# Performance work log

Hardware: AMD Instinct MI355X
Metric: run time of the kernel (lower is better)

The kernel has to match this reference:

```python
import jax, jax.numpy as jnp
import numpy as np

FEAT_DIM = 512
NUM_HEADS = 8
HEAD_DIM = FEAT_DIM // NUM_HEADS


def setup_inputs() -> dict:
    key = jax.random.key(0)
    ks = jax.random.split(key, 10)
    B, T, D = 4, 2048, FEAT_DIM
    scale = 1.0 / np.sqrt(D)
    inp = {
        "x_current": jax.random.normal(ks[0], (B, T, D), jnp.float32),
        "x_past": jax.random.normal(ks[1], (B, T, D), jnp.float32),
        "wq": jax.random.normal(ks[2], (D, D), jnp.float32) * scale,
        "bq": jnp.zeros((D,), jnp.float32),
        "wk": jax.random.normal(ks[3], (D, D), jnp.float32) * scale,
        "bk": jnp.zeros((D,), jnp.float32),
        "wv": jax.random.normal(ks[4], (D, D), jnp.float32) * scale,
        "bv": jnp.zeros((D,), jnp.float32),
        "wo": jax.random.normal(ks[5], (D, D), jnp.float32) * scale,
        "bo": jnp.zeros((D,), jnp.float32),
    }
    return inp


def reference(x_current, x_past, wq, bq, wk, bk, wv, bv, wo, bo):
    B, T, D = x_current.shape
    H, Hd = NUM_HEADS, HEAD_DIM
    # QKV projections (torch Linear: x @ W.T + b)
    Q = (x_current @ wq.T + bq).reshape(B, T, H, Hd).transpose(0, 2, 1, 3)
    K = (x_past @ wk.T + bk).reshape(B, T, H, Hd).transpose(0, 2, 1, 3)
    V = (x_past @ wv.T + bv).reshape(B, T, H, Hd).transpose(0, 2, 1, 3)
    # scaled dot-product attention, full T x T scores as in the original
    scores = jnp.einsum("bhqd,bhkd->bhqk", Q, K) / jnp.sqrt(jnp.asarray(Hd, Q.dtype))
    attn = jax.nn.softmax(scores, axis=-1)
    out = jnp.einsum("bhqk,bhkd->bhqd", attn, V)
    out = out.transpose(0, 2, 1, 3).reshape(B, T, D)
    return out @ wo.T + bo
```

## Files before the change

### kernel.cpp

```cpp
#include <hip/hip_runtime.h>
#include <math.h>

#define BATCH 4
#define SEQ 2048
#define FEAT 512
#define NHEADS 8
#define HD 64
#define NROWS (BATCH*SEQ)
#define QSCALE 0.18033688011112042f

typedef __attribute__((ext_vector_type(4)))  float f32x4;
typedef __attribute__((ext_vector_type(16))) float f32x16;
typedef __attribute__((ext_vector_type(8)))  short s16x8;
typedef __attribute__((ext_vector_type(8)))  unsigned short u16x8;
typedef __attribute__((ext_vector_type(4)))  unsigned int u32x4;

#if __has_builtin(__builtin_amdgcn_exp2f)
#define EX2(x) __builtin_amdgcn_exp2f(x)
#else
#define EX2(x) __expf((x) * 0.6931471805599453f)
#endif

static __device__ __forceinline__ unsigned short f2bf(float x) {
  unsigned int u = __builtin_bit_cast(unsigned int, x);
  unsigned int r = (u + 0x7FFFu + ((u >> 16) & 1u)) >> 16;
  return (unsigned short)r;
}
static __device__ __forceinline__ float bf2f(unsigned short h) {
  unsigned int u = ((unsigned int)h) << 16;
  return __builtin_bit_cast(float, u);
}
static __device__ __forceinline__ void split2(float x, unsigned short& h, unsigned short& l) {
  h = f2bf(x);
  l = f2bf(x - bf2f(h));
}

static __device__ __forceinline__ void glds16(const unsigned short* g, unsigned short* l) {
  __builtin_amdgcn_global_load_lds(
      (const __attribute__((address_space(1))) unsigned int*)g,
      (__attribute__((address_space(3))) unsigned int*)l,
      16, 0, 0);
}

__global__ __launch_bounds__(256) void presplit(
    const float* __restrict__ wq, const float* __restrict__ wk,
    const float* __restrict__ wv, const float* __restrict__ wo,
    const float* __restrict__ xc, const float* __restrict__ xp,
    unsigned short* __restrict__ Wsp,
    unsigned short* __restrict__ Xchi, unsigned short* __restrict__ Xphi)
{
  const int bid = blockIdx.x;
  if (bid < 512) {
    const int mat = bid >> 7;
    const int chunk = ((bid & 127) * 256 + threadIdx.x) * 8;
    const float* src = (mat == 0) ? wq : (mat == 1) ? wk : (mat == 2) ? wv : wo;
    unsigned short* hi = Wsp + (size_t)mat * 524288;
    unsigned short* lo = hi + 262144;
    const f32x4 a = *reinterpret_cast<const f32x4*>(&src[chunk]);
    const f32x4 b = *reinterpret_cast<const f32x4*>(&src[chunk + 4]);
    u16x8 h8, l8;
#pragma unroll
    for (int i = 0; i < 4; ++i) { unsigned short hh, ll; split2(a[i], hh, ll); h8[i] = hh; l8[i] = ll; }
#pragma unroll
    for (int i = 0; i < 4; ++i) { unsigned short hh, ll; split2(b[i], hh, ll); h8[4 + i] = hh; l8[4 + i] = ll; }
    *reinterpret_cast<u16x8*>(&hi[chunk]) = h8;
    *reinterpret_cast<u16x8*>(&lo[chunk]) = l8;
  } else {
    const int i = bid - 512;
    const int half = i >> 11;
    const int ib = i & 2047;
    const float* src = half ? xp : xc;
    unsigned short* dst = half ? Xphi : Xchi;
    const int chunk = (ib * 256 + threadIdx.x) * 8;
    const f32x4 a = *reinterpret_cast<const f32x4*>(&src[chunk]);
    const f32x4 b = *reinterpret_cast<const f32x4*>(&src[chunk + 4]);
    u16x8 h8;
#pragma unroll
    for (int ii = 0; ii < 4; ++ii) h8[ii] = f2bf(a[ii]);
#pragma unroll
    for (int ii = 0; ii < 4; ++ii) h8[4 + ii] = f2bf(b[ii]);
    *reinterpret_cast<u16x8*>(&dst[chunk]) = h8;
  }
}

__global__ __launch_bounds__(256, 4) void qkv_proj(
    const unsigned short* __restrict__ Xchi, const unsigned short* __restrict__ Xphi,
    const unsigned short* __restrict__ Wsp,
    const float* __restrict__ bq, const float* __restrict__ bk,
    const float* __restrict__ bv,
    unsigned short* __restrict__ Qhi, unsigned short* __restrict__ Khi,
    unsigned short* __restrict__ Vthi)
{
  __shared__ unsigned short Xh[128 * 64];
  __shared__ unsigned short Whi[64 * 64], Wlo[64 * 64];

  const int z = blockIdx.z;
  const unsigned short* Xsrc = (z == 0) ? Xchi : Xphi;
  const unsigned short* Wh_g = Wsp + (size_t)z * 524288;
  const unsigned short* Wl_g = Wh_g + 262144;
  const float* Bp = (z == 0) ? bq : (z == 1) ? bk : bv;
  const float scale = (z == 0) ? QSCALE : 1.0f;

  const int tid  = threadIdx.x;
  const int lane = tid & 63;
  const int wave = tid >> 6;
  const int g = lane >> 4, j = lane & 15;
  const int wm = (wave >> 1) * 64;
  const int wn = (wave & 1) * 32;
  const int row0 = blockIdx.x * 128;
  const int col0 = blockIdx.y * 64;

  f32x4 acc[4][2];
#pragma unroll
  for (int mi = 0; mi < 4; ++mi)
#pragma unroll
    for (int ni = 0; ni < 2; ++ni) acc[mi][ni] = (f32x4)0.f;

  const int xrow = wave * 32 + (lane >> 3);
  const int xkg  = (lane & 7) ^ ((lane >> 3) & 7);
  const unsigned short* srcX = Xsrc + (size_t)(row0 + xrow) * FEAT + xkg * 8;
  const int wrow = wave * 16 + (lane >> 3);
  const unsigned short* srcWh = Wh_g + (size_t)(col0 + wrow) * FEAT + xkg * 8;
  const unsigned short* srcWl = Wl_g + (size_t)(col0 + wrow) * FEAT + xkg * 8;

  for (int kt = 0; kt < FEAT; kt += 64) {
    __syncthreads();
#pragma unroll
    for (int c = 0; c < 4; ++c)
      glds16(srcX + kt + c * 4096, &Xh[(wave * 32 + c * 8) * 64]);
    glds16(srcWh + kt,        &Whi[(wave * 16) * 64]);
    glds16(srcWh + kt + 4096, &Whi[(wave * 16 + 8) * 64]);
    glds16(srcWl + kt,        &Wlo[(wave * 16) * 64]);
    glds16(srcWl + kt + 4096, &Wlo[(wave * 16 + 8) * 64]);
    asm volatile("s_waitcnt vmcnt(0)" ::: "memory");
    __syncthreads();

#pragma unroll
    for (int c = 0; c < 2; ++c) {
      const int koff = c * 32 + g * 8;
      s16x8 ah[4], bh[2], bl[2];
#pragma unroll
      for (int mi = 0; mi < 4; ++mi) {
        const int r = wm + mi * 16 + j;
        const int el = r * 64 + (koff ^ ((r & 7) << 3));
        ah[mi] = *reinterpret_cast<const s16x8*>(&Xh[el]);
      }
#pragma unroll
      for (int ni = 0; ni < 2; ++ni) {
        const int r = wn + ni * 16 + j;
        const int el = r * 64 + (koff ^ ((r & 7) << 3));
        bh[ni] = *reinterpret_cast<const s16x8*>(&Whi[el]);
        bl[ni] = *reinterpret_cast<const s16x8*>(&Wlo[el]);
      }
#pragma unroll
      for (int mi = 0; mi < 4; ++mi)
#pragma unroll
        for (int ni = 0; ni < 2; ++ni) {
          acc[mi][ni] = __builtin_amdgcn_mfma_f32_16x16x32_bf16(ah[mi], bh[ni], acc[mi][ni], 0, 0, 0);
          acc[mi][ni] = __builtin_amdgcn_mfma_f32_16x16x32_bf16(ah[mi], bl[ni], acc[mi][ni], 0, 0, 0);
        }
    }
  }

  if (z < 2) {
    unsigned short* Out = (z == 0) ? Qhi : Khi;
#pragma unroll
    for (int ni = 0; ni < 2; ++ni) {
      const int colc = col0 + wn + ni * 16 + j;
      const float bj = Bp[colc];
      const int h = colc >> 6, hd = colc & 63;
#pragma unroll
      for (int mi = 0; mi < 4; ++mi)
#pragma unroll
        for (int r = 0; r < 4; ++r) {
          const int rowc = row0 + wm + mi * 16 + (g << 2) + r;
          const int b = rowc >> 11, t = rowc & 2047;
          const float v = (acc[mi][ni][r] + bj) * scale;
          Out[(((size_t)b * NHEADS + h) * SEQ + t) * HD + hd] = f2bf(v);
        }
    }
  } else {
    __syncthreads();
#pragma unroll
    for (int ni = 0; ni < 2; ++ni) {
      const int hdl = wn + ni * 16 + j;
      const float bj = Bp[col0 + hdl];
#pragma unroll
      for (int mi = 0; mi < 4; ++mi)
#pragma unroll
        for (int r = 0; r < 4; ++r) {
          const int lt = wm + mi * 16 + (g << 2) + r;
          const float v = acc[mi][ni][r] + bj;
          const int el = lt * 64 + (hdl ^ ((lt & 7) << 3));
          Xh[el] = f2bf(v);
        }
    }
    __syncthreads();
    const int b = row0 >> 11, h = col0 >> 6;
    const int tbase = row0 & 2047;
#pragma unroll
    for (int c = 0; c < 4; ++c) {
      const int chunk = c * 256 + tid;
      const int hd = chunk >> 4;
      const int t0 = (chunk & 15) * 8;
      u16x8 vh;
#pragma unroll
      for (int i = 0; i < 8; ++i) {
        const int p = t0 + i;
        const int lt = (p & ~15) | ((p & 3) + (((p >> 2) & 1) << 3) + (((p >> 3) & 1) << 2));
        const int el = lt * 64 + (hd ^ ((lt & 7) << 3));
        vh[i] = Xh[el];
      }
      const size_t off = (((size_t)b * NHEADS + h) * HD + hd) * SEQ + tbase + t0;
      *reinterpret_cast<u16x8*>(&Vthi[off]) = vh;
    }
  }
}

__global__ __launch_bounds__(256, 4) void out_proj(
    const unsigned short* __restrict__ AOhi,
    const unsigned short* __restrict__ Woh,  const unsigned short* __restrict__ Wol,
    const float* __restrict__ bias, float* __restrict__ out)
{
  __shared__ unsigned short Xh[64 * 64];
  __shared__ unsigned short Whi[64 * 64], Wlo[64 * 64];

  const int tid  = threadIdx.x;
  const int lane = tid & 63;
  const int wave = tid >> 6;
  const int g = lane >> 4, j = lane & 15;
  const int wm = (wave >> 1) * 32;
  const int wn = (wave & 1) * 32;
  const int row0 = blockIdx.x * 64;
  const int col0 = blockIdx.y * 64;

  f32x4 acc[2][2];
#pragma unroll
  for (int mi = 0; mi < 2; ++mi)
#pragma unroll
    for (int ni = 0; ni < 2; ++ni) acc[mi][ni] = (f32x4)0.f;

  const int arow = wave * 16 + (lane >> 3);
  const int akg  = (lane & 7) ^ ((lane >> 3) & 7);
  const unsigned short* srcA  = AOhi + (size_t)(row0 + arow) * FEAT + akg * 8;
  const unsigned short* srcWh = Woh + (size_t)(col0 + arow) * FEAT + akg * 8;
  const unsigned short* srcWl = Wol + (size_t)(col0 + arow) * FEAT + akg * 8;

  for (int kt = 0; kt < FEAT; kt += 64) {
    __syncthreads();
    glds16(srcA + kt,         &Xh[(wave * 16) * 64]);
    glds16(srcA + kt + 4096,  &Xh[(wave * 16 + 8) * 64]);
    glds16(srcWh + kt,        &Whi[(wave * 16) * 64]);
    glds16(srcWh + kt + 4096, &Whi[(wave * 16 + 8) * 64]);
    glds16(srcWl + kt,        &Wlo[(wave * 16) * 64]);
    glds16(srcWl + kt + 4096, &Wlo[(wave * 16 + 8) * 64]);
    asm volatile("s_waitcnt vmcnt(0)" ::: "memory");
    __syncthreads();

#pragma unroll
    for (int c = 0; c < 2; ++c) {
      const int koff = c * 32 + g * 8;
      s16x8 ah[2], bh[2], bl[2];
#pragma unroll
      for (int mi = 0; mi < 2; ++mi) {
        const int r = wm + mi * 16 + j;
        const int el = r * 64 + (koff ^ ((r & 7) << 3));
        ah[mi] = *reinterpret_cast<const s16x8*>(&Xh[el]);
      }
#pragma unroll
      for (int ni = 0; ni < 2; ++ni) {
        const int r = wn + ni * 16 + j;
        const int el = r * 64 + (koff ^ ((r & 7) << 3));
        bh[ni] = *reinterpret_cast<const s16x8*>(&Whi[el]);
        bl[ni] = *reinterpret_cast<const s16x8*>(&Wlo[el]);
      }
#pragma unroll
      for (int mi = 0; mi < 2; ++mi)
#pragma unroll
        for (int ni = 0; ni < 2; ++ni) {
          acc[mi][ni] = __builtin_amdgcn_mfma_f32_16x16x32_bf16(ah[mi], bh[ni], acc[mi][ni], 0, 0, 0);
          acc[mi][ni] = __builtin_amdgcn_mfma_f32_16x16x32_bf16(ah[mi], bl[ni], acc[mi][ni], 0, 0, 0);
        }
    }
  }

#pragma unroll
  for (int ni = 0; ni < 2; ++ni) {
    const int colc = col0 + wn + ni * 16 + j;
    const float bj = bias[colc];
#pragma unroll
    for (int mi = 0; mi < 2; ++mi)
#pragma unroll
      for (int r = 0; r < 4; ++r) {
        const int rowc = row0 + wm + mi * 16 + (g << 2) + r;
        out[(size_t)rowc * FEAT + colc] = acc[mi][ni][r] + bj;
      }
  }
}

__global__ __launch_bounds__(256, 3) void attn_pipe(
    const unsigned short* __restrict__ Qhi,
    const unsigned short* __restrict__ Khi,
    const unsigned short* __restrict__ Vthi,
    unsigned short* __restrict__ AOhi)
{
  __shared__ unsigned short Kh_s[3][4096];
  __shared__ unsigned short Vh_s[3][4096];
  __shared__ float bcast[4][32];

  const int tid = threadIdx.x, lane = tid & 63, wave = tid >> 6;
  const int hfl = lane >> 5;
  const int l31 = lane & 31;

  const int bid = blockIdx.x;
  const int swz = (bid & 7) * 64 + (bid >> 3);
  const int qt  = swz & 15;
  const int bh  = swz >> 4;
  const int b = bh >> 3, h = bh & 7;

  const int q0 = qt * 128 + wave * 32;
  const size_t kvbase = (size_t)bh * SEQ * HD;

  s16x8 qh[4];
  {
    const size_t qoff = kvbase + (size_t)(q0 + l31) * HD + hfl * 8;
#pragma unroll
    for (int c = 0; c < 4; ++c)
      qh[c] = *reinterpret_cast<const s16x8*>(&Qhi[qoff + c * 16]);
  }

  f32x16 oacc0 = (f32x16)0.f, oacc1 = (f32x16)0.f;
  float m = -INFINITY, lsum = 0.f;

  const int ck  = tid >> 3;
  const int ksl = (tid & 7) ^ (ck & 7);
  const unsigned short* sKh = Khi + kvbase + (size_t)ck * HD + ksl * 8;
  const int vr  = tid >> 3;
  const int vsl = (tid & 7) ^ (vr & 7);
  const int vhd = vr + (vsl >> 2) * 32;
  const int vk0 = (vsl & 3) * 8;
  const unsigned short* sVh = Vthi + kvbase + (size_t)vhd * SEQ + vk0;
  const int wq = wave * 512;

  const int krow = l31 * 64;
  const int ksw  = l31 & 7;

  auto stage = [&](int tt, int bi) {
    const size_t ko = (size_t)tt * 64 * HD;
    const int    vo = tt * 64;
    glds16(sKh + ko,           &Kh_s[bi][wq]);
    glds16(sKh + ko + 32 * HD, &Kh_s[bi][2048 + wq]);
    glds16(sVh + vo,           &Vh_s[bi][wq]);
    glds16(sVh + vo + 32,      &Vh_s[bi][2048 + wq]);
  };

  stage(0, 0);
  stage(1, 1);

  const int NT = SEQ / 64;
  int cur = 0;
  for (int t = 0; t < NT; ++t) {
    if (t < NT - 1) {
      asm volatile("s_waitcnt vmcnt(4)" ::: "memory");
    } else {
      asm volatile("s_waitcnt vmcnt(0)" ::: "memory");
    }
    __syncthreads();
    if (t + 2 < NT) {
      int nb = cur + 2; if (nb >= 3) nb -= 3;
      stage(t + 2, nb);
    }
    __builtin_amdgcn_sched_barrier(0);

#pragma unroll
    for (int sub = 0; sub < 2; ++sub) {
      const int sb = sub * 2048;

      s16x8 KH[4];
#pragma unroll
      for (int c = 0; c < 4; ++c) {
        const int idx = sb + krow + ((((c << 1) | hfl)) ^ ksw) * 8;
        KH[c] = *reinterpret_cast<const s16x8*>(&Kh_s[cur][idx]);
      }

      f32x16 st = (f32x16)0.f;
      __builtin_amdgcn_s_setprio(1);
#pragma unroll
      for (int c = 0; c < 4; ++c)
        st = __builtin_amdgcn_mfma_f32_32x32x16_bf16(KH[c], qh[c], st, 0, 0, 0);
      __builtin_amdgcn_s_setprio(0);

      s16x8 V0h[2], V1h[2];
#pragma unroll
      for (int c = 0; c < 2; ++c) {
        const int i0 = sb + krow + ((((c << 1) | hfl)) ^ ksw) * 8;
        const int i1 = sb + krow + (((4 | (c << 1) | hfl)) ^ ksw) * 8;
        V0h[c] = *reinterpret_cast<const s16x8*>(&Vh_s[cur][i0]);
        V1h[c] = *reinterpret_cast<const s16x8*>(&Vh_s[cur][i1]);
      }

      const float a0 = fmaxf(fmaxf(st[0], st[1]), st[2]);
      const float a1 = fmaxf(fmaxf(st[3], st[4]), st[5]);
      const float a2 = fmaxf(fmaxf(st[6], st[7]), st[8]);
      const float a3 = fmaxf(fmaxf(st[9], st[10]), st[11]);
      const float a4 = fmaxf(fmaxf(st[12], st[13]), st[14]);
      const float pm = fmaxf(fmaxf(fmaxf(a0, a1), a2),
                             fmaxf(fmaxf(a3, a4), st[15]));

      if (__any(pm > m + 8.f)) {
        const float pmf  = fmaxf(pm, __shfl_xor(pm, 32));
        const float mnew = fmaxf(m, pmf);
        const float corr = EX2(m - mnew);
        m = mnew; lsum *= corr;
        if (lane < 32) bcast[wave][l31] = corr;
        f32x4 c4[4];
#pragma unroll
        for (int rq = 0; rq < 4; ++rq)
          c4[rq] = *reinterpret_cast<const f32x4*>(&bcast[wave][rq * 8 + hfl * 4]);
#pragma unroll
        for (int r = 0; r < 16; ++r) {
          const float cc = c4[r >> 2][r & 3];
          oacc0[r] *= cc; oacc1[r] *= cc;
        }
      }

#pragma unroll
      for (int r = 0; r < 16; ++r) st[r] = EX2(st[r] - m);
      {
        float s0 = (st[0] + st[1]) + (st[2] + st[3]);
        float s1 = (st[4] + st[5]) + (st[6] + st[7]);
        float s2 = (st[8] + st[9]) + (st[10] + st[11]);
        float s3 = (st[12] + st[13]) + (st[14] + st[15]);
        lsum += (s0 + s1) + (s2 + s3);
      }

      unsigned int wh[8];
#pragma unroll
      for (int p = 0; p < 8; ++p)
        asm("v_cvt_pk_bf16_f32 %0, %1, %2" : "=v"(wh[p]) : "v"(st[2 * p]), "v"(st[2 * p + 1]));
      const s16x8 pa0h = __builtin_bit_cast(s16x8, (u32x4){wh[0], wh[1], wh[2], wh[3]});
      const s16x8 pa1h = __builtin_bit_cast(s16x8, (u32x4){wh[4], wh[5], wh[6], wh[7]});

      __builtin_amdgcn_s_setprio(1);
      oacc0 = __builtin_amdgcn_mfma_f32_32x32x16_bf16(pa0h, V0h[0], oacc0, 0, 0, 0);
      oacc0 = __builtin_amdgcn_mfma_f32_32x32x16_bf16(pa1h, V0h[1], oacc0, 0, 0, 0);
      oacc1 = __builtin_amdgcn_mfma_f32_32x32x16_bf16(pa0h, V1h[0], oacc1, 0, 0, 0);
      oacc1 = __builtin_amdgcn_mfma_f32_32x32x16_bf16(pa1h, V1h[1], oacc1, 0, 0, 0);
      __builtin_amdgcn_s_setprio(0);
    }

    cur += 1; if (cur >= 3) cur -= 3;
  }

  const float lf = lsum + __shfl_xor(lsum, 32);
  if (lane < 32) bcast[wave][l31] = 1.f / lf;
  __syncthreads();
  f32x4 i4[4];
#pragma unroll
  for (int rq = 0; rq < 4; ++rq)
    i4[rq] = *reinterpret_cast<const f32x4*>(&bcast[wave][rq * 8 + hfl * 4]);

#pragma unroll
  for (int r = 0; r < 16; ++r) {
    const int q = q0 + (r & 3) + 8 * (r >> 2) + 4 * hfl;
    const float inv = i4[r >> 2][r & 3];
    const size_t idx = ((size_t)b * SEQ + q) * FEAT + h * HD + l31;
    AOhi[idx]      = f2bf(oacc0[r] * inv);
    AOhi[idx + 32] = f2bf(oacc1[r] * inv);
  }
}

extern "C" void kernel_launch(void* const* d_in, const int* in_sizes, int n_in,
                              void* d_out, int out_size, void* d_ws, size_t ws_size,
                              hipStream_t stream) {
  const float* x_cur  = (const float*)d_in[0];
  const float* x_past = (const float*)d_in[1];
  const float* wq = (const float*)d_in[2];
  const float* bq = (const float*)d_in[3];
  const float* wk = (const float*)d_in[4];
  const float* bk = (const float*)d_in[5];
  const float* wv = (const float*)d_in[6];
  const float* bv = (const float*)d_in[7];
  const float* wo = (const float*)d_in[8];
  const float* bo = (const float*)d_in[9];
  float* out = (float*)d_out;

  const size_t n = (size_t)NROWS * FEAT;
  unsigned short* Qhi  = (unsigned short*)d_ws;
  unsigned short* Xchi = Qhi + n;
  unsigned short* Khi  = Qhi + 2 * n;
  unsigned short* Xphi = Qhi + 3 * n;
  unsigned short* Vthi = Qhi + 4 * n;
  unsigned short* Wsp  = Qhi + 5 * n;
  unsigned short* AOhi = Qhi + 6 * n;

  dim3 block(256);
  presplit<<<dim3(4608), block, 0, stream>>>(wq, wk, wv, wo, x_cur, x_past,
                                             Wsp, Xchi, Xphi);

  qkv_proj<<<dim3(NROWS / 128, FEAT / 64, 3), block, 0, stream>>>(
      Xchi, Xphi, Wsp, bq, bk, bv, Qhi, Khi, Vthi);

  attn_pipe<<<dim3(512), block, 0, stream>>>(Qhi, Khi, Vthi, AOhi);

  dim3 gout(NROWS / 64, FEAT / 64);
  out_proj<<<gout, block, 0, stream>>>(AOhi, Wsp + 3 * 524288,
                                       Wsp + 3 * 524288 + 262144, bo, out);
}
```

Baseline: 103.0 us.

## Split attention over two key halves and merge partial outputs in a new kernel

The attention kernel now splits the key sequence into two halves, launching twice as many blocks, each writing unnormalized bf16 partial outputs plus per-row max and sum. A new merge kernel combines the two partials using log-sum-exp weights and writes the normalized result. The triple-buffered, two-ahead K/V prefetch is replaced by a simple double buffer with a full wait and barrier each tile. This aims to fill more CUs on a 512-block grid, at the cost of an extra kernel launch, extra memory traffic, bf16 rounding of the unnormalized partials, and less load/compute overlap.

Result: slower. 110.5 us (+7.2%).

```diff
diff --git a/kernel.cpp b/kernel.cpp
--- a/kernel.cpp
+++ b/kernel.cpp
@@ -302,17 +302,19 @@
     const unsigned short* __restrict__ Qhi,
     const unsigned short* __restrict__ Khi,
     const unsigned short* __restrict__ Vthi,
-    unsigned short* __restrict__ AOhi)
+    unsigned short* __restrict__ AOp0, unsigned short* __restrict__ AOp1,
+    float* __restrict__ ML)
 {
-  __shared__ unsigned short Kh_s[3][4096];
-  __shared__ unsigned short Vh_s[3][4096];
+  __shared__ unsigned short Kh_s[2][4096];
+  __shared__ unsigned short Vh_s[2][4096];
   __shared__ float bcast[4][32];
 
   const int tid = threadIdx.x, lane = tid & 63, wave = tid >> 6;
   const int hfl = lane >> 5;
   const int l31 = lane & 31;
 
-  const int bid = blockIdx.x;
+  const int sp  = blockIdx.x >> 9;
+  const int bid = blockIdx.x & 511;
   const int swz = (bid & 7) * 64 + (bid >> 3);
   const int qt  = swz & 15;
   const int bh  = swz >> 4;
@@ -321,6 +323,10 @@
   const int q0 = qt * 128 + wave * 32;
   const size_t kvbase = (size_t)bh * SEQ * HD;
 
+  unsigned short* AOp = sp ? AOp1 : AOp0;
+  float* mlm = ML + sp * 131072;
+  float* mll = mlm + 65536;
+
   s16x8 qh[4];
   {
     const size_t qoff = kvbase + (size_t)(q0 + l31) * HD + hfl * 8;
@@ -332,14 +338,15 @@
   f32x16 oacc0 = (f32x16)0.f, oacc1 = (f32x16)0.f;
   float m = -INFINITY, lsum = 0.f;
 
+  const int keybase = sp * (SEQ / 2);
   const int ck  = tid >> 3;
   const int ksl = (tid & 7) ^ (ck & 7);
-  const unsigned short* sKh = Khi + kvbase + (size_t)ck * HD + ksl * 8;
+  const unsigned short* sKh = Khi + kvbase + (size_t)(keybase + ck) * HD + ksl * 8;
   const int vr  = tid >> 3;
   const int vsl = (tid & 7) ^ (vr & 7);
   const int vhd = vr + (vsl >> 2) * 32;
   const int vk0 = (vsl & 3) * 8;
-  const unsigned short* sVh = Vthi + kvbase + (size_t)vhd * SEQ + vk0;
+  const unsigned short* sVh = Vthi + kvbase + (size_t)vhd * SEQ + keybase + vk0;
   const int wq = wave * 512;
 
   const int krow = l31 * 64;
@@ -355,21 +362,13 @@
   };
 
   stage(0, 0);
-  stage(1, 1);
-
-  const int NT = SEQ / 64;
+  asm volatile("s_waitcnt vmcnt(0)" ::: "memory");
+  __syncthreads();
+
+  const int NT = (SEQ / 2) / 64;
   int cur = 0;
   for (int t = 0; t < NT; ++t) {
-    if (t < NT - 1) {
-      asm volatile("s_waitcnt vmcnt(4)" ::: "memory");
-    } else {
-      asm volatile("s_waitcnt vmcnt(0)" ::: "memory");
-    }
-    __syncthreads();
-    if (t + 2 < NT) {
-      int nb = cur + 2; if (nb >= 3) nb -= 3;
-      stage(t + 2, nb);
-    }
+    if (t + 1 < NT) stage(t + 1, cur ^ 1);
     __builtin_amdgcn_sched_barrier(0);
 
 #pragma unroll
@@ -449,25 +448,52 @@
       __builtin_amdgcn_s_setprio(0);
     }
 
-    cur += 1; if (cur >= 3) cur -= 3;
+    asm volatile("s_waitcnt vmcnt(0)" ::: "memory");
+    __syncthreads();
+    cur ^= 1;
   }
 
   const float lf = lsum + __shfl_xor(lsum, 32);
-  if (lane < 32) bcast[wave][l31] = 1.f / lf;
-  __syncthreads();
-  f32x4 i4[4];
-#pragma unroll
-  for (int rq = 0; rq < 4; ++rq)
-    i4[rq] = *reinterpret_cast<const f32x4*>(&bcast[wave][rq * 8 + hfl * 4]);
+  if (lane < 32) {
+    const int mlrow = (bh << 11) + q0 + l31;
+    mlm[mlrow] = m;
+    mll[mlrow] = lf;
+  }
 
 #pragma unroll
   for (int r = 0; r < 16; ++r) {
     const int q = q0 + (r & 3) + 8 * (r >> 2) + 4 * hfl;
-    const float inv = i4[r >> 2][r & 3];
     const size_t idx = ((size_t)b * SEQ + q) * FEAT + h * HD + l31;
-    AOhi[idx]      = f2bf(oacc0[r] * inv);
-    AOhi[idx + 32] = f2bf(oacc1[r] * inv);
-  }
+    AOp[idx]      = f2bf(oacc0[r]);
+    AOp[idx + 32] = f2bf(oacc1[r]);
+  }
+}
+
+__global__ __launch_bounds__(256) void attn_merge(
+    unsigned short* __restrict__ AOp0, const unsigned short* __restrict__ AOp1,
+    const float* __restrict__ ML)
+{
+  const int gid = blockIdx.x * 256 + threadIdx.x;
+  const int e0 = gid * 8;
+  const int b   = e0 >> 20;
+  const int rem = e0 & 1048575;
+  const int q   = rem >> 9;
+  const int d   = rem & 511;
+  const int h   = d >> 6;
+  const int mlrow = (((b << 3) + h) << 11) + q;
+  const float m0 = ML[mlrow],          l0 = ML[65536 + mlrow];
+  const float m1 = ML[131072 + mlrow], l1 = ML[196608 + mlrow];
+  const float M  = fmaxf(m0, m1);
+  const float w0 = EX2(m0 - M), w1 = EX2(m1 - M);
+  const float inv = 1.f / (w0 * l0 + w1 * l1);
+  const float a = w0 * inv, c = w1 * inv;
+  const u16x8 x = *reinterpret_cast<const u16x8*>(&AOp0[e0]);
+  const u16x8 y = *reinterpret_cast<const u16x8*>(&AOp1[e0]);
+  u16x8 o;
+#pragma unroll
+  for (int i = 0; i < 8; ++i)
+    o[i] = f2bf(a * bf2f(x[i]) + c * bf2f(y[i]));
+  *reinterpret_cast<u16x8*>(&AOp0[e0]) = o;
 }
 
 extern "C" void kernel_launch(void* const* d_in, const int* in_sizes, int n_in,
@@ -501,7 +527,10 @@
   qkv_proj<<<dim3(NROWS / 128, FEAT / 64, 3), block, 0, stream>>>(
       Xchi, Xphi, Wsp, bq, bk, bv, Qhi, Khi, Vthi);
 
-  attn_pipe<<<dim3(512), block, 0, stream>>>(Qhi, Khi, Vthi, AOhi);
+  attn_pipe<<<dim3(1024), block, 0, stream>>>(Qhi, Khi, Vthi,
+                                              AOhi, Xchi, (float*)Xphi);
+
+  attn_merge<<<dim3(2048), block, 0, stream>>>(AOhi, Xchi, (float*)Xphi);
 
   dim3 gout(NROWS / 64, FEAT / 64);
   out_proj<<<gout, block, 0, stream>>>(AOhi, Wsp + 3 * 524288,
```
